# Performance work log

Measured on AMD Instinct MI355X. Metric: run time of the kernel, lower is better.

## Reference

```python
import jax, jax.numpy as jnp
import numpy as np

DIM = 192
NUM_HEADS = 8
EPS = 1e-12  # F.normalize default eps


def setup_inputs() -> dict:
    key = jax.random.key(0)
    ks = jax.random.split(key, 6)
    b, c, h, w = 8, DIM, 128, 128
    scale = 1.0 / np.sqrt(DIM)  # conv2d default init scale (approx)
    return {
        "input": jax.random.normal(ks[0], (b, c, h, w), dtype=jnp.float32),
        "color": jax.random.normal(ks[1], (b, c, h, w), dtype=jnp.float32),
        "Wq": jax.random.normal(ks[2], (DIM, DIM), dtype=jnp.float32) * scale,
        "Wk": jax.random.normal(ks[3], (DIM, DIM), dtype=jnp.float32) * scale,
        "Wv": jax.random.normal(ks[4], (DIM, DIM), dtype=jnp.float32) * scale,
        "Wo": jax.random.normal(ks[5], (DIM, DIM), dtype=jnp.float32) * scale,
    }


def _proj(x, W):
    # 1x1 conv (bias=False) == channel GEMM: [b,c,h,w] x [out,c] -> [b,out,h,w]
    return jnp.einsum('bchw,oc->bohw', x, W)


def _l2norm(x):
    n = jnp.sqrt(jnp.sum(x * x, axis=-1, keepdims=True))
    return x / jnp.maximum(n, EPS)


def reference(input, color, Wq, Wk, Wv, Wo):
    b, c, h, w = input.shape
    head = NUM_HEADS
    dh = c // head
    hw = h * w
    # q from color, k/v from input
    q = _proj(color, Wq).reshape(b, head, dh, hw)
    k = _proj(input, Wk).reshape(b, head, dh, hw)
    v = _proj(input, Wv).reshape(b, head, dh, hw)
    q = _l2norm(q)
    k = _l2norm(k)
    # transposed (channel) attention: [b,head,dh,dh]
    attn = jnp.einsum('bhcn,bhdn->bhcd', q, k)
    attn = jax.nn.softmax(attn, axis=-1)
    out = jnp.einsum('bhcd,bhdn->bhcn', attn, v)  # [b,head,dh,hw]
    out = out.reshape(b, c, h, w)
    return _proj(out, Wo)
```

## Files before the change

### kernel.cpp

```cpp
#include <hip/hip_runtime.h>
#include <hip/hip_bf16.h>


typedef __attribute__((ext_vector_type(4))) float f32x4;
typedef __attribute__((ext_vector_type(16))) float f32x16;
typedef __attribute__((ext_vector_type(8))) short short8;

#define MFMA16(a, b, c) __builtin_amdgcn_mfma_f32_16x16x32_bf16((a), (b), (c), 0, 0, 0)
#define MFMA32(a, b, c) __builtin_amdgcn_mfma_f32_32x32x16_bf16((a), (b), (c), 0, 0, 0)

__device__ __forceinline__ unsigned int pack_rne(float a, float b) {
  unsigned int ua = __float_as_uint(a), ub = __float_as_uint(b);
  ua += 0x7fffu + ((ua >> 16) & 1u);
  ub += 0x7fffu + ((ub >> 16) & 1u);
  return (ua >> 16) | (ub & 0xffff0000u);
}
__device__ __forceinline__ unsigned short bf16u_rne(float x) {
  unsigned int u = __float_as_uint(x);
  u += 0x7fffu + ((u >> 16) & 1u);
  return (unsigned short)(u >> 16);
}
union S8U { short8 s; unsigned int u[4]; };
__device__ __forceinline__ short8 load_cvt8(const float* p) {
  f32x4 x = *(const f32x4*)p;
  f32x4 y = *(const f32x4*)(p + 4);
  S8U r;
  r.u[0] = pack_rne(x[0], x[1]);
  r.u[1] = pack_rne(x[2], x[3]);
  r.u[2] = pack_rne(y[0], y[1]);
  r.u[3] = pack_rne(y[2], y[3]);
  return r.s;
}

#define HW 16384
#define CDIM 192
#define NB 8
#define GSZ (CDIM * CDIM)
#define NREC 78
#define NPART 64
#define NCP 8
#define FSLOT 24576
#define FSKEW 64
#define BROW 80

__global__ void k0_wvt(const float* __restrict__ Wv, unsigned short* __restrict__ WvT) {
  int idx = blockIdx.x * 256 + threadIdx.x;
  if (idx < CDIM * CDIM) {
    int j = idx / CDIM, cp = idx % CDIM;
    WvT[idx] = bf16u_rne(Wv[(size_t)cp * CDIM + j]);
  }
}

__device__ __forceinline__ void stageC(const float* __restrict__ ib,
                                       const float* __restrict__ cb, int col0,
                                       char* fdst, int wave, int lane) {
#pragma unroll
  for (int i = 0; i < 2; ++i) {
    const int g = wave * 2 + i;
    const int tensor = g >= 12;
    const int row = (g - (tensor ? 12 : 0)) * 16 + (lane >> 2);
    const float* T = tensor ? cb : ib;
    const float* gp = T + (size_t)row * HW + col0 + (lane & 3) * 4;
    __builtin_amdgcn_global_load_lds(
        (const __attribute__((address_space(1))) void*)gp,
        (__attribute__((address_space(3))) void*)(fdst + g * 1024), 16, 0, 0);
  }
}

template <int P, int H>
__device__ __forceinline__ void pair_step32(const char* bb, f32x16* acc,
                                            int l31, int hi16, int kb) {
  constexpr int N0 = 12 - P;
  constexpr int I0 = H ? 7 : 0;
  constexpr int I1 = H ? 13 : 7;
  const short8 aP = *(const short8*)(bb + (P * 32 + l31) * BROW + hi16 + kb);
  short8 aQ = aP;
  if constexpr (I1 > N0)
    aQ = *(const short8*)(bb + ((11 - P) * 32 + l31) * BROW + hi16 + kb);
#pragma unroll
  for (int i = I0; i < I1; ++i) {
    const int ct = (i < N0) ? (P + i) : (i - N0 + 11 - P);
    const short8 bfr = *(const short8*)(bb + (ct * 32 + l31) * BROW + hi16 + kb);
    acc[i - I0] = MFMA32((i < N0) ? aP : aQ, bfr, acc[i - I0]);
  }
}

template <int P, int H>
__device__ __forceinline__ void pair_both(const char* bb, f32x16* acc,
                                          int l31, int hi16) {
  pair_step32<P, H>(bb, acc, l31, hi16, 0);
  pair_step32<P, H>(bb, acc, l31, hi16, 32);
}

__device__ __forceinline__ void pair_dispatch(int wave, const char* bb,
                                              f32x16* acc, int l31, int hi16) {
  switch (wave) {
    case 0: pair_both<0, 0>(bb, acc, l31, hi16); break;
    case 1: pair_both<0, 1>(bb, acc, l31, hi16); break;
    case 2: pair_both<1, 0>(bb, acc, l31, hi16); break;
    case 3: pair_both<1, 1>(bb, acc, l31, hi16); break;
    case 4: pair_both<2, 0>(bb, acc, l31, hi16); break;
    case 5: pair_both<2, 1>(bb, acc, l31, hi16); break;
    case 6: pair_both<3, 0>(bb, acc, l31, hi16); break;
    case 7: pair_both<3, 1>(bb, acc, l31, hi16); break;
    case 8: pair_both<4, 0>(bb, acc, l31, hi16); break;
    case 9: pair_both<4, 1>(bb, acc, l31, hi16); break;
    case 10: pair_both<5, 0>(bb, acc, l31, hi16); break;
    default: pair_both<5, 1>(bb, acc, l31, hi16); break;
  }
}

__global__ __launch_bounds__(768) void gram2_k(const float* __restrict__ input,
                                               const float* __restrict__ color,
                                               unsigned long long* __restrict__ part) {
  __shared__ __align__(16) char fbuf[2][FSLOT + FSKEW];
  __shared__ __align__(16) char bbuf[384 * BROW];
  const int tid = threadIdx.x, wave = tid >> 6, lane = tid & 63;
  const int l31 = lane & 31, hi16 = (lane >> 5) * 16;
  const int strip = blockIdx.x, b = blockIdx.y;
  const float* ib = input + (size_t)b * CDIM * HW;
  const float* cb = color + (size_t)b * CDIM * HW;
  const int ch0 = strip * NCP * 2;

  f32x16 acc[7];
#pragma unroll
  for (int s = 0; s < 7; ++s)
#pragma unroll
    for (int c = 0; c < 16; ++c) acc[s][c] = 0.f;

  stageC(ib, cb, (ch0 + 0) * 16, fbuf[0], wave, lane);
  stageC(ib, cb, (ch0 + 1) * 16, fbuf[1], wave, lane);

#pragma unroll 1
  for (int cp = 0; cp < NCP; ++cp) {
    __syncthreads();
    {
      const char* sA = fbuf[0];
      const char* sB = fbuf[1];
#pragma unroll
      for (int u0 = 0; u0 < 2; ++u0) {
        const int u = tid + u0 * 768;
        const int zr = u >> 2, sub = u & 3;
        const char* src = (sub < 2 ? sA : sB) + zr * 64 + (sub & 1) * 32;
        f32x4 x = *(const f32x4*)src;
        f32x4 y = *(const f32x4*)(src + 16);
        S8U pk;
        pk.u[0] = pack_rne(x[0], x[1]);
        pk.u[1] = pack_rne(x[2], x[3]);
        pk.u[2] = pack_rne(y[0], y[1]);
        pk.u[3] = pack_rne(y[2], y[3]);
        *(short8*)(bbuf + zr * BROW + sub * 16) = pk.s;
      }
    }
    __syncthreads();
    if (cp + 1 < NCP) {
      stageC(ib, cb, (ch0 + 2 * cp + 2) * 16, fbuf[0], wave, lane);
      stageC(ib, cb, (ch0 + 2 * cp + 3) * 16, fbuf[1], wave, lane);
    }
    pair_dispatch(wave, bbuf, acc, l31, hi16);
  }

  unsigned long long* pbase = part + (size_t)(b * NPART + strip) * NREC * 256;
  const int p = wave >> 1, H = wave & 1;
  const int Rbase = p * 13 + (H ? 7 : 0);
  const int NT = H ? 6 : 7;
#pragma unroll
  for (int s = 0; s < 7; ++s) {
    if (s < NT) {
#pragma unroll
      for (int j = 0; j < 4; ++j) {
        const unsigned long long pk =
            (unsigned long long)pack_rne(acc[s][4 * j], acc[s][4 * j + 1]) |
            ((unsigned long long)pack_rne(acc[s][4 * j + 2], acc[s][4 * j + 3]) << 32);
        pbase[((size_t)(Rbase + s) * 4 + j) * 64 + lane] = pk;
      }
    }
  }
}

template <int NP>
__global__ __launch_bounds__(256) void reduce_k(const unsigned long long* __restrict__ part,
                                                float* __restrict__ G) {
  const int b = blockIdx.y, T = blockIdx.x;
  const int j = threadIdx.x >> 6, lane = threadIdx.x & 63;
  const unsigned long long* p0 =
      part + ((size_t)b * NP * NREC + T) * 256 + j * 64 + lane;
  float s0 = 0.f, s1 = 0.f, s2 = 0.f, s3 = 0.f;
#pragma unroll
  for (int s = 0; s < NP; ++s) {
    const unsigned long long v = p0[(size_t)s * NREC * 256];
    const unsigned int lo = (unsigned int)v, hi = (unsigned int)(v >> 32);
    s0 += __uint_as_float(lo << 16);
    s1 += __uint_as_float(lo & 0xffff0000u);
    s2 += __uint_as_float(hi << 16);
    s3 += __uint_as_float(hi & 0xffff0000u);
  }
  const int p = T / 13, i = T % 13;
  const int N0 = 12 - p;
  const int rt = (i < N0) ? p : 11 - p;
  const int ct = (i < N0) ? p + i : i - N0 + 11 - p;
  const int hi5 = lane >> 5, col = lane & 31;
  const int zc = ct * 32 + col;
  const float sums[4] = {s0, s1, s2, s3};
#pragma unroll
  for (int m = 0; m < 4; ++m) {
    const int zr = rt * 32 + m + 8 * j + 4 * hi5;
    int type, gr, gc;
    if (zc < 192) { type = 2; gr = zr; gc = zc; }
    else if (zr < 192) { type = 0; gr = zr; gc = zc - 192; }
    else { type = 1; gr = zr - 192; gc = zc - 192; }
    float* Gm = G + ((size_t)type * NB + b) * GSZ;
    Gm[(size_t)gr * CDIM + gc] = sums[m];
    if (type != 0 && rt != ct) Gm[(size_t)gc * CDIM + gr] = sums[m];
  }
}

__global__ __launch_bounds__(256) void k2a(const float* __restrict__ G,
                                           const float* __restrict__ Wq,
                                           const float* __restrict__ Wk,
                                           float* __restrict__ A_pre,
                                           float* __restrict__ nqk) {
  const int b = blockIdx.x, type = blockIdx.y;
  __shared__ __align__(16) unsigned short Hs[192][200];
  const int tid = threadIdx.x, wave = tid >> 6, lane = tid & 63;
  const int l15 = lane & 15, lg = lane >> 4, row0 = wave * 48;
  const float* W1 = (type == 2) ? Wk : Wq;
  const float* Gm = G + ((size_t)type * NB + b) * GSZ;

  f32x4 acc[3][12];
#pragma unroll
  for (int t = 0; t < 3; t++)
#pragma unroll
    for (int j = 0; j < 12; j++) acc[t][j] = (f32x4){0.f, 0.f, 0.f, 0.f};

  for (int ks = 0; ks < 192; ks += 32) {
    short8 afr[3];
#pragma unroll
    for (int t = 0; t < 3; t++)
      afr[t] = load_cvt8(W1 + (size_t)(row0 + t * 16 + l15) * CDIM + ks + lg * 8);
#pragma unroll
    for (int tj = 0; tj < 12; tj++) {
      short8 bfr = load_cvt8(Gm + (size_t)(tj * 16 + l15) * CDIM + ks + lg * 8);
#pragma unroll
      for (int t = 0; t < 3; t++) acc[t][tj] = MFMA16(afr[t], bfr, acc[t][tj]);
    }
  }
#pragma unroll
  for (int t = 0; t < 3; t++)
#pragma unroll
    for (int tj = 0; tj < 12; tj++)
#pragma unroll
      for (int r = 0; r < 4; r++)
        Hs[row0 + t * 16 + lg * 4 + r][tj * 16 + l15] = bf16u_rne(acc[t][tj][r]);
  __syncthreads();

  if (type == 0) {
    f32x4 a2[3][12];
#pragma unroll
    for (int t = 0; t < 3; t++)
#pragma unroll
      for (int j = 0; j < 12; j++) a2[t][j] = (f32x4){0.f, 0.f, 0.f, 0.f};
    for (int ks = 0; ks < 192; ks += 32) {
      short8 afr[3];
#pragma unroll
      for (int t = 0; t < 3; t++)
        afr[t] = *(const short8*)&Hs[row0 + t * 16 + l15][ks + lg * 8];
#pragma unroll
      for (int tj = 0; tj < 12; tj++) {
        short8 bfr = load_cvt8(Wk + (size_t)(tj * 16 + l15) * CDIM + ks + lg * 8);
#pragma unroll
        for (int t = 0; t < 3; t++) a2[t][tj] = MFMA16(afr[t], bfr, a2[t][tj]);
      }
    }
    float* Ab = A_pre + (size_t)b * GSZ;
#pragma unroll
    for (int t = 0; t < 3; t++)
#pragma unroll
      for (int tj = 0; tj < 12; tj++)
#pragma unroll
        for (int r = 0; r < 4; r++)
          Ab[(size_t)(row0 + t * 16 + lg * 4 + r) * CDIM + tj * 16 + l15] = a2[t][tj][r];
  } else {
    f32x4 a2[3];
#pragma unroll
    for (int t = 0; t < 3; t++) a2[t] = (f32x4){0.f, 0.f, 0.f, 0.f};
    for (int ks = 0; ks < 192; ks += 32) {
#pragma unroll
      for (int t = 0; t < 3; t++) {
        short8 afr = *(const short8*)&Hs[row0 + t * 16 + l15][ks + lg * 8];
        short8 bfr = load_cvt8(W1 + (size_t)(row0 + t * 16 + l15) * CDIM + ks + lg * 8);
        a2[t] = MFMA16(afr, bfr, a2[t]);
      }
    }
    float* dst = nqk + ((size_t)(type - 1) * NB + b) * CDIM;
#pragma unroll
    for (int t = 0; t < 3; t++)
#pragma unroll
      for (int r = 0; r < 4; r++)
        if (lg * 4 + r == l15) dst[row0 + t * 16 + l15] = a2[t][r];
  }
}

__global__ void k2b(const float* __restrict__ A_pre, const float* __restrict__ nqk,
                    float* __restrict__ attnw) {
  const int b = blockIdx.x, tid = threadIdx.x;
  const int h = tid >> 5, r = tid & 31;
  if (r >= 24) return;
  const float* Ab = A_pre + (size_t)b * GSZ;
  const float* nq = nqk + (size_t)b * CDIM;
  const float* nk = nqk + (size_t)(NB + b) * CDIM;
  const int c = h * 24 + r;
  const float qn = rsqrtf(fmaxf(nq[c], 1e-24f));
  float e[24];
  float mx = -1e30f;
#pragma unroll
  for (int d = 0; d < 24; d++) {
    float kn = rsqrtf(fmaxf(nk[h * 24 + d], 1e-24f));
    float l = Ab[(size_t)c * CDIM + h * 24 + d] * qn * kn;
    e[d] = l;
    mx = fmaxf(mx, l);
  }
  float s = 0.f;
#pragma unroll
  for (int d = 0; d < 24; d++) {
    float x = __expf(e[d] - mx);
    e[d] = x;
    s += x;
  }
  const float inv = 1.0f / s;
  float* dst = attnw + (((size_t)b * NB + h) * 24 + r) * 24;
#pragma unroll
  for (int d = 0; d < 24; d++) dst[d] = e[d] * inv;
}

__global__ __launch_bounds__(256) void k3(const float* __restrict__ attnw,
                                          const float* __restrict__ Wo,
                                          const unsigned short* __restrict__ WvT,
                                          unsigned short* __restrict__ Pbf) {
  const int b = blockIdx.x;
  __shared__ __align__(16) unsigned short AT[192][200];
  __shared__ __align__(16) unsigned short Ms[192][200];
  const int tid = threadIdx.x, wave = tid >> 6, lane = tid & 63;
  const int l15 = lane & 15, lg = lane >> 4, row0 = wave * 48;

  unsigned int* ATu = (unsigned int*)&AT[0][0];
  for (int i = tid; i < 192 * 100; i += 256) ATu[i] = 0u;
  __syncthreads();
  const float* at = attnw + (size_t)b * NB * 24 * 24;
  for (int i = tid; i < 4608; i += 256) {
    int h = i / 576, rem = i % 576, c = rem / 24, d = rem % 24;
    AT[h * 24 + d][h * 24 + c] = bf16u_rne(at[(h * 24 + c) * 24 + d]);
  }
  __syncthreads();

  f32x4 acc[3][12];
#pragma unroll
  for (int t = 0; t < 3; t++)
#pragma unroll
    for (int j = 0; j < 12; j++) acc[t][j] = (f32x4){0.f, 0.f, 0.f, 0.f};
  for (int ks = 0; ks < 192; ks += 32) {
    short8 afr[3];
#pragma unroll
    for (int t = 0; t < 3; t++)
      afr[t] = load_cvt8(Wo + (size_t)(row0 + t * 16 + l15) * CDIM + ks + lg * 8);
#pragma unroll
    for (int tj = 0; tj < 12; tj++) {
      short8 bfr = *(const short8*)&AT[tj * 16 + l15][ks + lg * 8];
#pragma unroll
      for (int t = 0; t < 3; t++) acc[t][tj] = MFMA16(afr[t], bfr, acc[t][tj]);
    }
  }
#pragma unroll
  for (int t = 0; t < 3; t++)
#pragma unroll
    for (int tj = 0; tj < 12; tj++)
#pragma unroll
      for (int r = 0; r < 4; r++)
        Ms[row0 + t * 16 + lg * 4 + r][tj * 16 + l15] = bf16u_rne(acc[t][tj][r]);
  __syncthreads();

  f32x4 a2[3][12];
#pragma unroll
  for (int t = 0; t < 3; t++)
#pragma unroll
    for (int j = 0; j < 12; j++) a2[t][j] = (f32x4){0.f, 0.f, 0.f, 0.f};
  for (int ks = 0; ks < 192; ks += 32) {
    short8 afr[3];
#pragma unroll
    for (int t = 0; t < 3; t++)
      afr[t] = *(const short8*)&Ms[row0 + t * 16 + l15][ks + lg * 8];
#pragma unroll
    for (int tj = 0; tj < 12; tj++) {
      short8 bfr = *(const short8*)(WvT + (size_t)(tj * 16 + l15) * CDIM + ks + lg * 8);
#pragma unroll
      for (int t = 0; t < 3; t++) a2[t][tj] = MFMA16(afr[t], bfr, a2[t][tj]);
    }
  }
  unsigned short* Pb = Pbf + (size_t)b * GSZ;
#pragma unroll
  for (int t = 0; t < 3; t++)
#pragma unroll
    for (int tj = 0; tj < 12; tj++)
#pragma unroll
      for (int r = 0; r < 4; r++)
        Pb[(size_t)(row0 + t * 16 + lg * 4 + r) * CDIM + tj * 16 + l15] = bf16u_rne(a2[t][tj][r]);
}

__global__ __launch_bounds__(256) void kD(const unsigned short* __restrict__ Pbf,
                                          const float* __restrict__ input,
                                          float* __restrict__ out) {
  const int nchunk = blockIdx.x, b = blockIdx.y;
  const int n0 = nchunk * 128;
  __shared__ __align__(16) char BsT[128 * 384];
  const int tid = threadIdx.x, wave = tid >> 6, lane = tid & 63;
  const int l15 = lane & 15, lg = lane >> 4, row0 = wave * 48;

  {
    const int n4 = (tid & 31) * 4;
    const int kb0 = (tid >> 5) * 4;
    const float* src = input + (size_t)b * CDIM * HW + n0 + n4;
    f32x4 w[24];
#pragma unroll
    for (int rnd = 0; rnd < 6; ++rnd)
#pragma unroll
      for (int j = 0; j < 4; ++j)
        w[rnd * 4 + j] = *(const f32x4*)(src + (size_t)(kb0 + rnd * 32 + j) * HW);
    __builtin_amdgcn_sched_barrier(0);
    char* bsb = BsT;
#pragma unroll
    for (int rnd = 0; rnd < 6; ++rnd) {
      const int kb = kb0 + rnd * 32;
#pragma unroll
      for (int i = 0; i < 4; ++i) {
        const int n = n4 + i;
        unsigned long long pk =
            (unsigned long long)pack_rne(w[rnd * 4 + 0][i], w[rnd * 4 + 1][i]) |
            ((unsigned long long)pack_rne(w[rnd * 4 + 2][i], w[rnd * 4 + 3][i]) << 32);
        *(unsigned long long*)(bsb + n * 384 + ((kb * 2) ^ ((n & 7) << 4))) = pk;
      }
    }
  }
  __syncthreads();

  f32x4 acc[3][8];
#pragma unroll
  for (int t = 0; t < 3; t++)
#pragma unroll
    for (int j = 0; j < 8; j++) acc[t][j] = (f32x4){0.f, 0.f, 0.f, 0.f};

  const unsigned short* Pb = Pbf + (size_t)b * GSZ;
#pragma unroll 2
  for (int ks = 0; ks < 6; ks++) {
    short8 afr[3];
#pragma unroll
    for (int t = 0; t < 3; t++)
      afr[t] = *(const short8*)(Pb + (size_t)(row0 + t * 16 + l15) * CDIM + ks * 32 + lg * 8);
#pragma unroll
    for (int tn = 0; tn < 8; tn++) {
      const int n = tn * 16 + l15;
      short8 bfr = *(const short8*)(BsT + n * 384 + ((ks * 64 + lg * 16) ^ ((n & 7) << 4)));
#pragma unroll
      for (int t = 0; t < 3; t++) acc[t][tn] = MFMA16(afr[t], bfr, acc[t][tn]);
    }
  }
  float* ob = out + (size_t)b * CDIM * HW + n0;
#pragma unroll
  for (int t = 0; t < 3; t++)
#pragma unroll
    for (int tn = 0; tn < 8; tn++)
#pragma unroll
      for (int r = 0; r < 4; r++) {
        const int m = row0 + t * 16 + lg * 4 + r;
        ob[(size_t)m * HW + tn * 16 + l15] = acc[t][tn][r];
      }
}

extern "C" void kernel_launch(void* const* d_in, const int* in_sizes, int n_in,
                              void* d_out, int out_size, void* d_ws, size_t ws_size,
                              hipStream_t stream) {
  const float* input = (const float*)d_in[0];
  const float* color = (const float*)d_in[1];
  const float* Wq = (const float*)d_in[2];
  const float* Wk = (const float*)d_in[3];
  const float* Wv = (const float*)d_in[4];
  const float* Wo = (const float*)d_in[5];
  float* out = (float*)d_out;
  char* ws = (char*)d_ws;

  const size_t OFF_G = 0;
  const size_t OFF_APRE = 3538944;
  const size_t OFF_NQK = OFF_APRE + 1179648;
  const size_t OFF_ATT = OFF_NQK + 12288;
  const size_t OFF_WVT = OFF_ATT + 147456;
  const size_t OFF_PBF = OFF_WVT + 73728;

  float* G = (float*)(ws + OFF_G);
  float* A_pre = (float*)(ws + OFF_APRE);
  float* nqk = (float*)(ws + OFF_NQK);
  float* attnw = (float*)(ws + OFF_ATT);
  unsigned short* WvT = (unsigned short*)(ws + OFF_WVT);
  unsigned short* Pbf = (unsigned short*)(ws + OFF_PBF);

  unsigned long long* part = (unsigned long long*)d_out;

  k0_wvt<<<dim3(144), dim3(256), 0, stream>>>(Wv, WvT);
  gram2_k<<<dim3(NPART, NB), dim3(768), 0, stream>>>(input, color, part);
  reduce_k<NPART><<<dim3(NREC, NB), dim3(256), 0, stream>>>(part, G);
  k2a<<<dim3(NB, 3), dim3(256), 0, stream>>>(G, Wq, Wk, A_pre, nqk);
  k2b<<<dim3(NB), dim3(256), 0, stream>>>(A_pre, nqk, attnw);
  k3<<<dim3(NB), dim3(256), 0, stream>>>(attnw, Wo, WvT, Pbf);
  kD<<<dim3(HW / 128, NB), dim3(256), 0, stream>>>(Pbf, input, out);
}
```

Measured before the change: 204.9 us.

## Prefetch gram inputs into registers instead of LDS double-buffer, halve partial count

The gram kernel drops the async global-to-LDS fp32 staging buffers and instead has each thread load its 32-column slices of input and color rows directly into registers, converting to bf16 and writing the packed tile to LDS once per iteration. The number of spatial partial strips is halved, so each block processes twice as many column chunks and the cross-strip reduction has fewer partials. This frees a large amount of LDS, which may allow more resident blocks, and removes an LDS round-trip. The cost is more registers held across the MFMA phase, and global loads whose latency is covered only by the MFMA work of one iteration. Fewer blocks also means less grid parallelism.

```diff
diff --git a/kernel.cpp b/kernel.cpp
--- a/kernel.cpp
+++ b/kernel.cpp
@@ -37,10 +37,8 @@
 #define NB 8
 #define GSZ (CDIM * CDIM)
 #define NREC 78
-#define NPART 64
-#define NCP 8
-#define FSLOT 24576
-#define FSKEW 64
+#define NPART 32
+#define NCP 16
 #define BROW 80
 
 __global__ void k0_wvt(const float* __restrict__ Wv, unsigned short* __restrict__ WvT) {
@@ -48,22 +46,6 @@
   if (idx < CDIM * CDIM) {
     int j = idx / CDIM, cp = idx % CDIM;
     WvT[idx] = bf16u_rne(Wv[(size_t)cp * CDIM + j]);
-  }
-}
-
-__device__ __forceinline__ void stageC(const float* __restrict__ ib,
-                                       const float* __restrict__ cb, int col0,
-                                       char* fdst, int wave, int lane) {
-#pragma unroll
-  for (int i = 0; i < 2; ++i) {
-    const int g = wave * 2 + i;
-    const int tensor = g >= 12;
-    const int row = (g - (tensor ? 12 : 0)) * 16 + (lane >> 2);
-    const float* T = tensor ? cb : ib;
-    const float* gp = T + (size_t)row * HW + col0 + (lane & 3) * 4;
-    __builtin_amdgcn_global_load_lds(
-        (const __attribute__((address_space(1))) void*)gp,
-        (__attribute__((address_space(3))) void*)(fdst + g * 1024), 16, 0, 0);
   }
 }
 
@@ -113,13 +95,13 @@
 __global__ __launch_bounds__(768) void gram2_k(const float* __restrict__ input,
                                                const float* __restrict__ color,
                                                unsigned long long* __restrict__ part) {
-  __shared__ __align__(16) char fbuf[2][FSLOT + FSKEW];
   __shared__ __align__(16) char bbuf[384 * BROW];
   const int tid = threadIdx.x, wave = tid >> 6, lane = tid & 63;
   const int l31 = lane & 31, hi16 = (lane >> 5) * 16;
   const int strip = blockIdx.x, b = blockIdx.y;
-  const float* ib = input + (size_t)b * CDIM * HW;
-  const float* cb = color + (size_t)b * CDIM * HW;
+  const int row = tid >> 2, sub = tid & 3;
+  const float* ip = input + (size_t)b * CDIM * HW + (size_t)row * HW;
+  const float* cp_ = color + (size_t)b * CDIM * HW + (size_t)row * HW;
   const int ch0 = strip * NCP * 2;
 
   f32x16 acc[7];
@@ -128,34 +110,38 @@
 #pragma unroll
     for (int c = 0; c < 16; ++c) acc[s][c] = 0.f;
 
-  stageC(ib, cb, (ch0 + 0) * 16, fbuf[0], wave, lane);
-  stageC(ib, cb, (ch0 + 1) * 16, fbuf[1], wave, lane);
+  f32x4 vi0, vi1, vc0, vc1;
+  {
+    const int colf = (ch0 + (sub >> 1)) * 16 + (sub & 1) * 8;
+    vi0 = *(const f32x4*)(ip + colf);
+    vi1 = *(const f32x4*)(ip + colf + 4);
+    vc0 = *(const f32x4*)(cp_ + colf);
+    vc1 = *(const f32x4*)(cp_ + colf + 4);
+  }
 
 #pragma unroll 1
-  for (int cp = 0; cp < NCP; ++cp) {
+  for (int cpi = 0; cpi < NCP; ++cpi) {
     __syncthreads();
     {
-      const char* sA = fbuf[0];
-      const char* sB = fbuf[1];
-#pragma unroll
-      for (int u0 = 0; u0 < 2; ++u0) {
-        const int u = tid + u0 * 768;
-        const int zr = u >> 2, sub = u & 3;
-        const char* src = (sub < 2 ? sA : sB) + zr * 64 + (sub & 1) * 32;
-        f32x4 x = *(const f32x4*)src;
-        f32x4 y = *(const f32x4*)(src + 16);
-        S8U pk;
-        pk.u[0] = pack_rne(x[0], x[1]);
-        pk.u[1] = pack_rne(x[2], x[3]);
-        pk.u[2] = pack_rne(y[0], y[1]);
-        pk.u[3] = pack_rne(y[2], y[3]);
-        *(short8*)(bbuf + zr * BROW + sub * 16) = pk.s;
-      }
+      S8U pk;
+      pk.u[0] = pack_rne(vi0[0], vi0[1]);
+      pk.u[1] = pack_rne(vi0[2], vi0[3]);
+      pk.u[2] = pack_rne(vi1[0], vi1[1]);
+      pk.u[3] = pack_rne(vi1[2], vi1[3]);
+      *(short8*)(bbuf + row * BROW + sub * 16) = pk.s;
+      pk.u[0] = pack_rne(vc0[0], vc0[1]);
+      pk.u[1] = pack_rne(vc0[2], vc0[3]);
+      pk.u[2] = pack_rne(vc1[0], vc1[1]);
+      pk.u[3] = pack_rne(vc1[2], vc1[3]);
+      *(short8*)(bbuf + (192 + row) * BROW + sub * 16) = pk.s;
     }
     __syncthreads();
-    if (cp + 1 < NCP) {
-      stageC(ib, cb, (ch0 + 2 * cp + 2) * 16, fbuf[0], wave, lane);
-      stageC(ib, cb, (ch0 + 2 * cp + 3) * 16, fbuf[1], wave, lane);
+    if (cpi + 1 < NCP) {
+      const int colf = (ch0 + 2 * (cpi + 1) + (sub >> 1)) * 16 + (sub & 1) * 8;
+      vi0 = *(const f32x4*)(ip + colf);
+      vi1 = *(const f32x4*)(ip + colf + 4);
+      vc0 = *(const f32x4*)(cp_ + colf);
+      vc1 = *(const f32x4*)(cp_ + colf + 4);
     }
     pair_dispatch(wave, bbuf, acc, l31, hi16);
   }
```

Result: faster. 181.0 us (-11.7%).
